# Kernel optimization log

Hardware: AMD Instinct MI355X
Metric: run time of the kernel (lower is better)

Reference implementation:

```python
import jax, jax.numpy as jnp
import numpy as np

MARKET_DIM, VELOCITY_DIM, AGENT_STATE_DIM = 20, 10, 10
RUNNER_DIM, POSITION_DIM, MAX_RUNNERS = 24, 8, 30
RUNNER_INPUT_DIM = RUNNER_DIM + POSITION_DIM            # 32
MARKET_TOTAL_DIM = MARKET_DIM + VELOCITY_DIM + AGENT_STATE_DIM  # 40
OBS_DIM = MARKET_DIM + VELOCITY_DIM + MAX_RUNNERS * RUNNER_DIM + AGENT_STATE_DIM + MAX_RUNNERS * POSITION_DIM  # 1000
TD_IDX = MARKET_DIM + (VELOCITY_DIM - 4)                # 26
B, T = 256, 64
MLP_H, LSTM_H = 128, 256
LSTM_IN = MLP_H + 2 * MLP_H                             # 384


def setup_inputs() -> dict:
    key = jax.random.key(0)
    ks = jax.random.split(key, 32)

    def w(k, o, i):
        return (jax.random.normal(k, (o, i), jnp.float32) / np.sqrt(i)).astype(jnp.float32)

    z = lambda n: jnp.zeros((n,), jnp.float32)
    return dict(
        obs=jax.random.normal(ks[0], (B, T, OBS_DIM), jnp.float32),
        # runner encoder: 32 -> 128 -> 128 -> 128
        re_w0=w(ks[1], MLP_H, RUNNER_INPUT_DIM), re_b0=z(MLP_H),
        re_w1=w(ks[2], MLP_H, MLP_H), re_b1=z(MLP_H),
        re_w2=w(ks[3], MLP_H, MLP_H), re_b2=z(MLP_H),
        # market encoder: 40 -> 128 -> 128 -> 128
        me_w0=w(ks[4], MLP_H, MARKET_TOTAL_DIM), me_b0=z(MLP_H),
        me_w1=w(ks[5], MLP_H, MLP_H), me_b1=z(MLP_H),
        me_w2=w(ks[6], MLP_H, MLP_H), me_b2=z(MLP_H),
        # TimeLSTM cell (single layer)
        W_ih=w(ks[7], 4 * LSTM_H, LSTM_IN), b_ih=z(4 * LSTM_H),
        W_hh=w(ks[8], 4 * LSTM_H, LSTM_H),
        W_dt=jnp.zeros((LSTM_H,), jnp.float32),
        # actor head: 384 -> 128 -> 2
        a_w0=w(ks[9], MLP_H, MLP_H + LSTM_H), a_b0=z(MLP_H),
        a_w1=w(ks[10], 2, MLP_H) * 0.01, a_b1=z(2),
        # critic head: 256 -> 128 -> 1
        c_w0=w(ks[11], MLP_H, LSTM_H), c_b0=z(MLP_H),
        c_w1=w(ks[12], 1, MLP_H), c_b1=z(1),
        log_std=jnp.zeros((MAX_RUNNERS * 2,), jnp.float32),
    )


def _mlp3(x, w0, b0, w1, b1, w2, b2):
    x = jax.nn.relu(x @ w0.T + b0)
    x = jax.nn.relu(x @ w1.T + b1)
    return x @ w2.T + b2


def _mlp2(x, w0, b0, w1, b1):
    return jax.nn.relu(x @ w0.T + b0) @ w1.T + b1


def reference(obs,
              re_w0, re_b0, re_w1, re_b1, re_w2, re_b2,
              me_w0, me_b0, me_w1, me_b1, me_w2, me_b2,
              W_ih, b_ih, W_hh, W_dt,
              a_w0, a_b0, a_w1, a_b1,
              c_w0, c_b0, c_w1, c_b1,
              log_std):
    b, t, _ = obs.shape
    of = obs.reshape(b * t, -1)
    market = of[:, :MARKET_DIM]
    vel = of[:, MARKET_DIM:MARKET_DIM + VELOCITY_DIM]
    rs = MARKET_DIM + VELOCITY_DIM
    re_ = rs + MAX_RUNNERS * RUNNER_DIM
    runners = of[:, rs:re_].reshape(b * t, MAX_RUNNERS, RUNNER_DIM)
    agent = of[:, re_:re_ + AGENT_STATE_DIM]
    ps = re_ + AGENT_STATE_DIM
    pos = of[:, ps:ps + MAX_RUNNERS * POSITION_DIM].reshape(b * t, MAX_RUNNERS, POSITION_DIM)

    market_feats = jnp.concatenate([market, vel, agent], axis=-1)        # (BT, 40)
    runner_feats = jnp.concatenate([runners, pos], axis=-1)              # (BT, R, 32)

    market_emb = _mlp3(market_feats, me_w0, me_b0, me_w1, me_b1, me_w2, me_b2)  # (BT, 128)
    runner_embs = _mlp3(runner_feats, re_w0, re_b0, re_w1, re_b1, re_w2, re_b2)  # (BT, R, 128)
    r_mean = runner_embs.mean(axis=1)
    r_max = runner_embs.max(axis=1)

    lstm_in = jnp.concatenate([market_emb, r_mean, r_max], axis=-1).reshape(b, t, LSTM_IN)
    dt = of[:, TD_IDX].reshape(b, t)

    h0 = jnp.zeros((b, LSTM_H), obs.dtype)
    c0 = jnp.zeros_like(h0)

    def step(hc, xs):
        h, c = hc
        x, d = xs                                           # (B, 384), (B,)
        gates = x @ W_ih.T + b_ih + h @ W_hh.T              # (B, 4H)
        i, f, g, o = jnp.split(gates, 4, axis=-1)
        f = f + W_dt * d[:, None]                           # time-modulated forget gate
        i, f, o = jax.nn.sigmoid(i), jax.nn.sigmoid(f), jax.nn.sigmoid(o)
        g = jnp.tanh(g)
        c_new = f * c + i * g
        h_new = o * jnp.tanh(c_new)
        return (h_new, c_new), None

    (h, c), _ = jax.lax.scan(step, (h0, c0), (lstm_in.transpose(1, 0, 2), dt.T))
    lstm_out = h  # layer_norm disabled -> identity

    runner_last = runner_embs.reshape(b, t, MAX_RUNNERS, MLP_H)[:, -1]   # (B, R, 128)
    actor_in = jnp.concatenate(
        [runner_last, jnp.broadcast_to(lstm_out[:, None, :], (b, MAX_RUNNERS, LSTM_H))], axis=-1)
    action_mean = _mlp2(actor_in, a_w0, a_b0, a_w1, a_b1).reshape(b, MAX_RUNNERS * 2)
    action_log_std = jnp.broadcast_to(log_std, action_mean.shape)
    value = _mlp2(lstm_out, c_w0, c_b0, c_w1, c_b1)                      # (B, 1)
    return action_mean, action_log_std, value, h, c
```

## Files before the change

kernel.cpp:

```cpp
#include <hip/hip_runtime.h>
#include <hip/hip_bf16.h>
#include <math.h>

#define Bn 256
#define Tn 64
#define OBSD 1000
#define NR 30
#define HD 128
#define LH 256
#define LIN 384
#define TDI 26

#define AM_OFF 0
#define ALS_OFF 15360
#define V_OFF 30720
#define H_OFF 30976
#define C_OFF 96512

typedef unsigned short u16;
typedef short bf16x8 __attribute__((ext_vector_type(8)));
typedef float f32x4 __attribute__((ext_vector_type(4)));

__device__ __forceinline__ float sigm(float x){ return 1.f/(1.f+__expf(-x)); }
__device__ __forceinline__ float tanhfast(float x){
    float ax = fabsf(x);
    float e = __expf(2.f*ax);
    float t = 1.f - 2.f/(e+1.f);
    return copysignf(t, x);
}

__device__ __forceinline__ u16 f2b(float f){
    union { __hip_bfloat16 h; u16 u; } cv;
    cv.h = __float2bfloat16(f);
    return cv.u;
}

__device__ __forceinline__ bf16x8 ld_b128_sys(const u16* p){
    bf16x8 r;
    asm volatile("global_load_dwordx4 %0, %1, off sc0 sc1"
                 : "=v"(r) : "v"(p) : "memory");
    return r;
}
__device__ __forceinline__ void st_b16_sys(u16* p, unsigned v){
    asm volatile("global_store_short %0, %1, off sc0 sc1"
                 :: "v"(p), "v"(v) : "memory");
}

#define MFMA(a,b,c) __builtin_amdgcn_mfma_f32_16x16x32_bf16(a,b,c,0,0,0)

__device__ __forceinline__ void pack_one(
    const float* __restrict__ src, u16* __restrict__ dst,
    int N, int K, int Kpad, int t)
{
    if (t >= N*Kpad) return;
    int j = t / Kpad, k = t - j*Kpad;
    float v = (k < K) ? src[j*K + k] : 0.f;
    int ntile = j>>4, jr = j&15, kc = k>>5, ko = k&31;
    int lane = ((ko>>3)<<4) | jr, elem = ko&7;
    int KC = Kpad>>5;
    dst[(size_t)(((ntile*KC + kc)*64) + lane)*8 + elem] = f2b(v);
}

__device__ __forceinline__ void pack_gi_one(
    const float* __restrict__ src, u16* __restrict__ dst, int K, int t)
{
    int KC = K >> 5;
    if (t >= 1024*K) return;
    int n = t / K, k = t - n*K;
    int nt = n>>4, jr = n&15;
    int jg = nt>>2, g = nt&3;
    float v = src[(size_t)(g*256 + jg*16 + jr)*K + k];
    int kc = k>>5, ko = k&31;
    int lane = ((ko>>3)<<4) | jr, e = ko&7;
    dst[(size_t)(((nt*KC + kc)*64) + lane)*8 + e] = f2b(v);
}

__global__ __launch_bounds__(256) void k_setup(
    const float* __restrict__ re_w0, u16* __restrict__ pw0,
    const float* __restrict__ re_w1, u16* __restrict__ pw1,
    const float* __restrict__ re_w2, u16* __restrict__ pw2,
    const float* __restrict__ me_w0, u16* __restrict__ pm0,
    const float* __restrict__ me_w1, u16* __restrict__ pm1,
    const float* __restrict__ me_w2, u16* __restrict__ pm2,
    const float* __restrict__ W_ih,  u16* __restrict__ pwih,
    const float* __restrict__ W_hh,  u16* __restrict__ pwhh,
    const float* __restrict__ obs,   float* __restrict__ dtv,
    unsigned int* __restrict__ flags)
{
    int blk = blockIdx.x, tid = threadIdx.x;
    if (blk < 16){            pack_one(re_w0, pw0, 128, 32, 32,  blk*256 + tid); }
    else if (blk < 80){       pack_one(re_w1, pw1, 128,128,128, (blk-16)*256 + tid); }
    else if (blk < 144){      pack_one(re_w2, pw2, 128,128,128, (blk-80)*256 + tid); }
    else if (blk < 176){      pack_one(me_w0, pm0, 128, 40, 64, (blk-144)*256 + tid); }
    else if (blk < 240){      pack_one(me_w1, pm1, 128,128,128, (blk-176)*256 + tid); }
    else if (blk < 304){      pack_one(me_w2, pm2, 128,128,128, (blk-240)*256 + tid); }
    else if (blk < 1840){     pack_gi_one(W_ih, pwih, 384, (blk-304)*256 + tid); }
    else if (blk < 2864){     pack_gi_one(W_hh, pwhh, 256, (blk-1840)*256 + tid); }
    else if (blk < 2928){
        int idx = (blk-2864)*256 + tid;
        int b = idx >> 6, t = idx & 63;
        dtv[t*256 + b] = obs[(size_t)idx*OBSD + TDI];
    } else {
        flags[(blk-2928)*256 + tid] = 0u;
    }
}

__global__ __launch_bounds__(256) void k_embed_market(
    const float* __restrict__ obs,
    const u16* __restrict__ pw0, const float* __restrict__ re_b0,
    const u16* __restrict__ pw1, const float* __restrict__ re_b1,
    const u16* __restrict__ pw2, const float* __restrict__ re_b2,
    const u16* __restrict__ pm0, const float* __restrict__ me_b0,
    const u16* __restrict__ pm1, const float* __restrict__ me_b1,
    const u16* __restrict__ pm2, const float* __restrict__ me_b2,
    u16* __restrict__ li_bf, float* __restrict__ runner_last)
{
    __shared__ __align__(16) u16 smem[19968];
    __shared__ float bsf[384];

    int blk = blockIdx.x, tid = threadIdx.x;
    int lane = tid & 63, wv = tid >> 6;
    int lr = lane & 15, lk = lane >> 4;
    f32x4 zero = {0.f,0.f,0.f,0.f};

    if (blk < 8192){
        u16* xr   = smem;
        u16* act1 = smem + 2560;
        u16* act2 = smem + 11264;
        float* bs0 = bsf, *bs1 = bsf+128, *bs2 = bsf+256;

        int bt0 = blk*2;

        for (int idx=tid; idx<2048; idx+=256){
            int r = idx>>5, k = idx&31;
            int sb = r>>5, rr = r&31;
            const float* row = obs + (size_t)(bt0+sb)*OBSD;
            float v = 0.f;
            if (rr < 30) v = (k<24) ? row[30 + rr*24 + k] : row[760 + rr*8 + (k-24)];
            xr[r*40 + k] = f2b(v);
        }
        if (tid < 128){ bs0[tid]=re_b0[tid]; bs1[tid]=re_b1[tid]; bs2[tid]=re_b2[tid]; }
        __syncthreads();

        f32x4 d[4][2];

        {
            bf16x8 a0[4];
            #pragma unroll
            for (int m=0;m<4;m++) a0[m] = *(const bf16x8*)(xr + (m*16+lr)*40 + lk*8);
            #pragma unroll
            for (int ns=0; ns<2; ns++){
                int n = 2*wv + ns;
                bf16x8 b = *(const bf16x8*)(pw0 + (size_t)(n*64 + lane)*8);
                #pragma unroll
                for (int m=0;m<4;m++) d[m][ns] = MFMA(a0[m], b, zero);
            }
        }
        #pragma unroll
        for (int m=0;m<4;m++)
            #pragma unroll
            for (int ns=0;ns<2;ns++){
                int col = (2*wv+ns)*16 + lr;
                float bias = bs0[col];
                #pragma unroll
                for (int r=0;r<4;r++)
                    act1[(m*16+lk*4+r)*136 + col] = f2b(fmaxf(d[m][ns][r] + bias, 0.f));
            }
        __syncthreads();

        #pragma unroll
        for (int m=0;m<4;m++)
            #pragma unroll
            for (int ns=0;ns<2;ns++) d[m][ns] = zero;
        #pragma unroll
        for (int kc=0; kc<4; kc++){
            bf16x8 am[4];
            #pragma unroll
            for (int m=0;m<4;m++) am[m] = *(const bf16x8*)(act1 + (m*16+lr)*136 + kc*32 + lk*8);
            #pragma unroll
            for (int ns=0; ns<2; ns++){
                int n = 2*wv + ns;
                bf16x8 b = *(const bf16x8*)(pw1 + (size_t)((n*4 + kc)*64 + lane)*8);
                #pragma unroll
                for (int m=0;m<4;m++) d[m][ns] = MFMA(am[m], b, d[m][ns]);
            }
        }
        #pragma unroll
        for (int m=0;m<4;m++)
            #pragma unroll
            for (int ns=0;ns<2;ns++){
                int col = (2*wv+ns)*16 + lr;
                float bias = bs1[col];
                #pragma unroll
                for (int r=0;r<4;r++)
                    act2[(m*16+lk*4+r)*136 + col] = f2b(fmaxf(d[m][ns][r] + bias, 0.f));
            }
        __syncthreads();

        #pragma unroll
        for (int m=0;m<4;m++)
            #pragma unroll
            for (int ns=0;ns<2;ns++) d[m][ns] = zero;
        #pragma unroll
        for (int kc=0; kc<4; kc++){
            bf16x8 am[4];
            #pragma unroll
            for (int m=0;m<4;m++) am[m] = *(const bf16x8*)(act2 + (m*16+lr)*136 + kc*32 + lk*8);
            #pragma unroll
            for (int ns=0; ns<2; ns++){
                int n = 2*wv + ns;
                bf16x8 b = *(const bf16x8*)(pw2 + (size_t)((n*4 + kc)*64 + lane)*8);
                #pragma unroll
                for (int m=0;m<4;m++) d[m][ns] = MFMA(am[m], b, d[m][ns]);
            }
        }

        u16* li0 = li_bf + (size_t)bt0*LIN;
        u16* li1 = li_bf + (size_t)(bt0+1)*LIN;
        bool last1 = (((bt0+1) & 63) == 63);
        int bb1 = (bt0+1) >> 6;

        #pragma unroll
        for (int ns=0; ns<2; ns++){
            int col = (2*wv+ns)*16 + lr;
            float bias = bs2[col];
            float vals[4][4];
            float s0=0.f, m0=-3.4e38f, s1=0.f, m1=-3.4e38f;
            #pragma unroll
            for (int m=0;m<4;m++)
                #pragma unroll
                for (int r=0;r<4;r++){
                    int rw = m*16 + lk*4 + r;
                    float v = d[m][ns][r] + bias;
                    vals[m][r] = v;
                    if (m < 2){
                        bool ok = rw < 30;
                        s0 += ok ? v : 0.f;
                        m0 = fmaxf(m0, ok ? v : -3.4e38f);
                    } else {
                        bool ok = (rw-32) < 30;
                        s1 += ok ? v : 0.f;
                        m1 = fmaxf(m1, ok ? v : -3.4e38f);
                    }
                }
            s0 += __shfl_xor(s0, 16); s0 += __shfl_xor(s0, 32);
            m0 = fmaxf(m0, __shfl_xor(m0, 16)); m0 = fmaxf(m0, __shfl_xor(m0, 32));
            s1 += __shfl_xor(s1, 16); s1 += __shfl_xor(s1, 32);
            m1 = fmaxf(m1, __shfl_xor(m1, 16)); m1 = fmaxf(m1, __shfl_xor(m1, 32));
            if (lk == 0){
                li0[128 + col] = f2b(s0 * (1.0f/30.0f));
                li0[256 + col] = f2b(m0);
            }
            if (lk == 1){
                li1[128 + col] = f2b(s1 * (1.0f/30.0f));
                li1[256 + col] = f2b(m1);
            }
            if (last1){
                #pragma unroll
                for (int m=2;m<4;m++)
                    #pragma unroll
                    for (int r=0;r<4;r++){
                        int rw = m*16 + lk*4 + r - 32;
                        if (rw < 30) runner_last[(size_t)bb1*3840 + rw*128 + col] = vals[m][r];
                    }
            }
        }
    } else {
        u16* xm  = smem;
        u16* ma1 = smem + 2304;
        u16* ma2 = smem + 6656;
        float* bs0 = bsf, *bs1 = bsf+128, *bs2 = bsf+256;

        int bt0 = (blk - 8192)*32;
        for (int idx=tid; idx<2048; idx+=256){
            int r = idx>>6, k = idx&63;
            const float* row = obs + (size_t)(bt0+r)*OBSD;
            float v = 0.f;
            if (k < 30) v = row[k];
            else if (k < 40) v = row[720 + k];
            xm[r*72 + k] = f2b(v);
        }
        if (tid < 128){ bs0[tid]=me_b0[tid]; bs1[tid]=me_b1[tid]; bs2[tid]=me_b2[tid]; }
        __syncthreads();

        f32x4 d[2][2];

        #pragma unroll
        for (int m=0;m<2;m++)
            #pragma unroll
            for (int ns=0;ns<2;ns++) d[m][ns] = zero;
        #pragma unroll
        for (int kc=0; kc<2; kc++){
            bf16x8 a0 = *(const bf16x8*)(xm + lr*72      + kc*32 + lk*8);
            bf16x8 a1 = *(const bf16x8*)(xm + (16+lr)*72 + kc*32 + lk*8);
            #pragma unroll
            for (int ns=0; ns<2; ns++){
                int n = 2*wv + ns;
                bf16x8 b = *(const bf16x8*)(pm0 + (size_t)((n*2 + kc)*64 + lane)*8);
                d[0][ns] = MFMA(a0, b, d[0][ns]);
                d[1][ns] = MFMA(a1, b, d[1][ns]);
            }
        }
        #pragma unroll
        for (int m=0;m<2;m++)
            #pragma unroll
            for (int ns=0;ns<2;ns++){
                int col = (2*wv+ns)*16 + lr;
                float bias = bs0[col];
                #pragma unroll
                for (int r=0;r<4;r++){
                    int rw = m*16 + lk*4 + r;
                    ma1[rw*136 + col] = f2b(fmaxf(d[m][ns][r] + bias, 0.f));
                }
            }
        __syncthreads();

        #pragma unroll
        for (int m=0;m<2;m++)
            #pragma unroll
            for (int ns=0;ns<2;ns++) d[m][ns] = zero;
        #pragma unroll
        for (int kc=0; kc<4; kc++){
            bf16x8 a0 = *(const bf16x8*)(ma1 + lr*136      + kc*32 + lk*8);
            bf16x8 a1 = *(const bf16x8*)(ma1 + (16+lr)*136 + kc*32 + lk*8);
            #pragma unroll
            for (int ns=0; ns<2; ns++){
                int n = 2*wv + ns;
                bf16x8 b = *(const bf16x8*)(pm1 + (size_t)((n*4 + kc)*64 + lane)*8);
                d[0][ns] = MFMA(a0, b, d[0][ns]);
                d[1][ns] = MFMA(a1, b, d[1][ns]);
            }
        }
        #pragma unroll
        for (int m=0;m<2;m++)
            #pragma unroll
            for (int ns=0;ns<2;ns++){
                int col = (2*wv+ns)*16 + lr;
                float bias = bs1[col];
                #pragma unroll
                for (int r=0;r<4;r++){
                    int rw = m*16 + lk*4 + r;
                    ma2[rw*136 + col] = f2b(fmaxf(d[m][ns][r] + bias, 0.f));
                }
            }
        __syncthreads();

        #pragma unroll
        for (int m=0;m<2;m++)
            #pragma unroll
            for (int ns=0;ns<2;ns++) d[m][ns] = zero;
        #pragma unroll
        for (int kc=0; kc<4; kc++){
            bf16x8 a0 = *(const bf16x8*)(ma2 + lr*136      + kc*32 + lk*8);
            bf16x8 a1 = *(const bf16x8*)(ma2 + (16+lr)*136 + kc*32 + lk*8);
            #pragma unroll
            for (int ns=0; ns<2; ns++){
                int n = 2*wv + ns;
                bf16x8 b = *(const bf16x8*)(pm2 + (size_t)((n*4 + kc)*64 + lane)*8);
                d[0][ns] = MFMA(a0, b, d[0][ns]);
                d[1][ns] = MFMA(a1, b, d[1][ns]);
            }
        }
        #pragma unroll
        for (int m=0;m<2;m++)
            #pragma unroll
            for (int ns=0;ns<2;ns++){
                int col = (2*wv+ns)*16 + lr;
                float bias = bs2[col];
                #pragma unroll
                for (int r=0;r<4;r++){
                    int rw = m*16 + lk*4 + r;
                    li_bf[(size_t)(bt0+rw)*LIN + col] = f2b(d[m][ns][r] + bias);
                }
            }
    }
}

__global__ __launch_bounds__(256) void k_xw(
    const u16* __restrict__ A, const u16* __restrict__ pwih,
    const float* __restrict__ b_ih, float* __restrict__ xw)
{
    __shared__ __align__(16) u16 bsh[48*512];

    int tid = threadIdx.x;
    int lane = tid & 63, wv = tid >> 6;
    int lr = lane & 15, lk = lane >> 4;
    int r0 = blockIdx.x*128 + wv*32;

    bf16x8 a[2][12];
    #pragma unroll
    for (int m=0;m<2;m++)
        #pragma unroll
        for (int kc=0;kc<12;kc++)
            a[m][kc] = *(const bf16x8*)(A + (size_t)(r0+m*16+lr)*384 + kc*32 + lk*8);

    for (int jg=0; jg<16; jg++){
        {
            const bf16x8* src = (const bf16x8*)(pwih + (size_t)jg*48*512);
            bf16x8* dst = (bf16x8*)bsh;
            #pragma unroll
            for (int i=0;i<12;i++)
                dst[tid + i*256] = src[tid + i*256];
        }
        __syncthreads();

        f32x4 acc[2][4];
        #pragma unroll
        for (int g=0; g<4; g++){
            float bias = b_ih[g*256 + jg*16 + lr];
            f32x4 v = {bias,bias,bias,bias};
            acc[0][g]=v; acc[1][g]=v;
        }
        #pragma unroll
        for (int kc=0; kc<12; kc++){
            bf16x8 b0 = *(const bf16x8*)(bsh + (size_t)((0*12+kc)*64+lane)*8);
            bf16x8 b1 = *(const bf16x8*)(bsh + (size_t)((1*12+kc)*64+lane)*8);
            bf16x8 b2 = *(const bf16x8*)(bsh + (size_t)((2*12+kc)*64+lane)*8);
            bf16x8 b3 = *(const bf16x8*)(bsh + (size_t)((3*12+kc)*64+lane)*8);
            #pragma unroll
            for (int m=0;m<2;m++){
                acc[m][0] = MFMA(a[m][kc], b0, acc[m][0]);
                acc[m][1] = MFMA(a[m][kc], b1, acc[m][1]);
                acc[m][2] = MFMA(a[m][kc], b2, acc[m][2]);
                acc[m][3] = MFMA(a[m][kc], b3, acc[m][3]);
            }
        }
        #pragma unroll
        for (int m=0;m<2;m++)
            #pragma unroll
            for (int r=0;r<4;r++){
                int row = r0 + m*16 + lk*4 + r;
                int trow = (row & 63)*256 + (row >> 6);
                float4 pk;
                pk.x = acc[m][0][r]; pk.y = acc[m][1][r];
                pk.z = acc[m][2][r]; pk.w = acc[m][3][r];
                *(float4*)(xw + ((size_t)trow*256 + jg*16 + lr)*4) = pk;
            }
        __syncthreads();
    }
}

__global__ __launch_bounds__(256,1) void k_lstm_pair(
    const float* __restrict__ xw, const u16* __restrict__ pwhh,
    const float* __restrict__ W_dt, const float* __restrict__ dtv,
    u16* __restrict__ hb0, u16* __restrict__ hb1,
    float* __restrict__ hout, float* __restrict__ cout,
    unsigned int* __restrict__ flags)
{
    int tid = threadIdx.x;
    int lane = tid & 63, wv = tid >> 6;
    int lr = lane & 15, lk = lane >> 4;
    int blk = blockIdx.x;
    int p = blk >> 1, hf = blk & 1;
    int bb0 = p*16;
    int jg0 = hf*8 + wv*2;

    bf16x8 bfr[2][4][8];
    #pragma unroll
    for (int jl=0;jl<2;jl++)
        #pragma unroll
        for (int g=0;g<4;g++)
            #pragma unroll
            for (int kc=0;kc<8;kc++)
                bfr[jl][g][kc] = *(const bf16x8*)(pwhh + (size_t)((((jg0+jl)*4+g)*8+kc)*64+lane)*8);

    float wdt0 = W_dt[jg0*16 + lr];
    float wdt1 = W_dt[(jg0+1)*16 + lr];

    float cst[2][4] = {{0.f,0.f,0.f,0.f},{0.f,0.f,0.f,0.f}};
    bf16x8 a[8];
    #pragma unroll
    for (int kc=0;kc<8;kc++) a[kc] = (bf16x8)(short)0;

    int bth = bb0 + lk*4;

    float4 xwn[2][4];
    #pragma unroll
    for (int jl=0;jl<2;jl++)
        #pragma unroll
        for (int r=0;r<4;r++)
            xwn[jl][r] = *(const float4*)(xw + ((size_t)(bth+r)*256 + (jg0+jl)*16 + lr)*4);
    float4 dtn = *(const float4*)(dtv + bth);

    f32x4 acc[2][4];
    #pragma unroll
    for (int jl=0;jl<2;jl++){
        f32x4 v0, v1, v2, v3;
        #pragma unroll
        for (int r=0;r<4;r++){
            v0[r] = xwn[jl][r].x; v1[r] = xwn[jl][r].y;
            v2[r] = xwn[jl][r].z; v3[r] = xwn[jl][r].w;
        }
        acc[jl][0] = v0; acc[jl][1] = v1; acc[jl][2] = v2; acc[jl][3] = v3;
    }

    unsigned int* myflag   = &flags[blk*64];
    unsigned int* partflag = &flags[(blk^1)*64];

    for (int t=0; t<64; t++){
        asm volatile("s_waitcnt vmcnt(0)" ::: "memory");
        __builtin_amdgcn_sched_barrier(0);

        #pragma unroll
        for (int kc=0; kc<8; kc++){
            #pragma unroll
            for (int jl=0;jl<2;jl++){
                acc[jl][0] = MFMA(a[kc], bfr[jl][0][kc], acc[jl][0]);
                acc[jl][1] = MFMA(a[kc], bfr[jl][1][kc], acc[jl][1]);
                acc[jl][2] = MFMA(a[kc], bfr[jl][2][kc], acc[jl][2]);
                acc[jl][3] = MFMA(a[kc], bfr[jl][3][kc], acc[jl][3]);
            }
        }

        u16* hw = (t&1) ? hb1 : hb0;
        #pragma unroll
        for (int jl=0;jl<2;jl++){
            float wdt = jl ? wdt1 : wdt0;
            int jcol = (jg0+jl)*16 + lr;
            #pragma unroll
            for (int r=0;r<4;r++){
                float dd = (r==0)?dtn.x:(r==1)?dtn.y:(r==2)?dtn.z:dtn.w;
                float gi = sigm(acc[jl][0][r]);
                float gf = sigm(acc[jl][1][r] + wdt*dd);
                float gg = tanhfast(acc[jl][2][r]);
                float go = sigm(acc[jl][3][r]);
                float cn = fmaf(gf, cst[jl][r], gi*gg);
                cst[jl][r] = cn;
                float hv = go * tanhfast(cn);
                if (t < 63){
                    st_b16_sys(hw + (size_t)(bth+r)*256 + jcol, (unsigned)f2b(hv));
                } else {
                    hout[(size_t)(bth+r)*256 + jcol] = hv;
                    cout[(size_t)(bth+r)*256 + jcol] = cn;
                }
            }
        }

        if (t < 63){
            asm volatile("s_waitcnt vmcnt(0)" ::: "memory");
            __syncthreads();
            if (tid == 0)
                __hip_atomic_store(myflag, (unsigned)(t+1),
                                   __ATOMIC_RELAXED, __HIP_MEMORY_SCOPE_SYSTEM);

            #pragma unroll
            for (int jl=0;jl<2;jl++)
                #pragma unroll
                for (int r=0;r<4;r++)
                    xwn[jl][r] = *(const float4*)(xw + ((size_t)((t+1)*256 + bth+r)*256 + (jg0+jl)*16 + lr)*4);
            dtn = *(const float4*)(dtv + (t+1)*256 + bth);

            if (lane == 0){
                while (__hip_atomic_load(partflag, __ATOMIC_RELAXED,
                                         __HIP_MEMORY_SCOPE_SYSTEM) < (unsigned)(t+1)) {}
            }
            __builtin_amdgcn_wave_barrier();

            const u16* hr = (t&1) ? hb1 : hb0;
            #pragma unroll
            for (int kc=0; kc<8; kc++)
                a[kc] = ld_b128_sys(hr + (size_t)(bb0+lr)*256 + kc*32 + lk*8);

            #pragma unroll
            for (int jl=0;jl<2;jl++){
                f32x4 v0, v1, v2, v3;
                #pragma unroll
                for (int r=0;r<4;r++){
                    v0[r] = xwn[jl][r].x; v1[r] = xwn[jl][r].y;
                    v2[r] = xwn[jl][r].z; v3[r] = xwn[jl][r].w;
                }
                acc[jl][0] = v0; acc[jl][1] = v1; acc[jl][2] = v2; acc[jl][3] = v3;
            }
        }
    }
}

__device__ __forceinline__ void dense30(
    const float* in, int istride,
    const float* __restrict__ W, int wstride, int K,
    const float* __restrict__ bias, const float* extra,
    float* outp, int ostride, bool relu, int j, int rh)
{
    float acc[15];
    #pragma unroll
    for (int i=0;i<15;i++) acc[i]=0.f;
    const float* w = W + j*wstride;
    for (int k=0;k<K;k+=4){
        float4 wv = *(const float4*)(w+k);
        #pragma unroll
        for (int i=0;i<15;i++){
            float4 xv = *(const float4*)(in + (rh+2*i)*istride + k);
            acc[i] = fmaf(wv.x,xv.x,acc[i]);
            acc[i] = fmaf(wv.y,xv.y,acc[i]);
            acc[i] = fmaf(wv.z,xv.z,acc[i]);
            acc[i] = fmaf(wv.w,xv.w,acc[i]);
        }
    }
    float bb = bias[j] + (extra ? extra[j] : 0.f);
    #pragma unroll
    for (int i=0;i<15;i++){
        float v = acc[i]+bb;
        outp[(rh+2*i)*ostride+j] = relu ? fmaxf(v,0.f) : v;
    }
}

__device__ __forceinline__ float dense1(
    const float* in, const float* __restrict__ W,
    const float* __restrict__ bias, int K, int j)
{
    const float* w = W + j*K;
    float s = 0.f;
    for (int k=0;k<K;k+=4){
        float4 wv = *(const float4*)(w+k);
        float4 xv = *(const float4*)(in+k);
        s = fmaf(wv.x,xv.x,s); s = fmaf(wv.y,xv.y,s);
        s = fmaf(wv.z,xv.z,s); s = fmaf(wv.w,xv.w,s);
    }
    return s + bias[j];
}

__global__ __launch_bounds__(256) void k_heads(
    const float* __restrict__ h, const float* __restrict__ cbuf,
    const float* __restrict__ rl,
    const float* __restrict__ a_w0, const float* __restrict__ a_b0,
    const float* __restrict__ a_w1, const float* __restrict__ a_b1,
    const float* __restrict__ c_w0, const float* __restrict__ c_b0,
    const float* __restrict__ c_w1, const float* __restrict__ c_b1,
    const float* __restrict__ log_std,
    float* __restrict__ out)
{
    __shared__ __align__(16) float hv[LH];
    __shared__ __align__(16) float rls[NR][HD];
    __shared__ __align__(16) float hid[NR][HD];
    __shared__ __align__(16) float dot2[HD];
    __shared__ __align__(16) float red[128];

    int b = blockIdx.x, tid = threadIdx.x;
    hv[tid] = h[b*LH + tid];
    for (int idx=tid; idx<NR*HD; idx+=256) rls[idx>>7][idx&127] = rl[(size_t)b*NR*HD + idx];
    __syncthreads();

    if (tid < 128){
        const float* w = a_w0 + tid*LIN + HD;
        float s = 0.f;
        for (int k=0;k<LH;k+=4){
            float4 wv = *(const float4*)(w+k);
            s = fmaf(wv.x,hv[k],s); s = fmaf(wv.y,hv[k+1],s);
            s = fmaf(wv.z,hv[k+2],s); s = fmaf(wv.w,hv[k+3],s);
        }
        dot2[tid] = s;
    }
    __syncthreads();

    int j = tid & 127, rh = tid >> 7;
    dense30(&rls[0][0], HD, a_w0, LIN, HD, a_b0, dot2, &hid[0][0], HD, true, j, rh);
    __syncthreads();

    if (tid < 60){
        int r = tid >> 1, o = tid & 1;
        const float* w = a_w1 + o*HD;
        float s = a_b1[o];
        for (int k=0;k<HD;k++) s = fmaf(hid[r][k], w[k], s);
        out[AM_OFF + b*60 + tid] = s;
        out[ALS_OFF + b*60 + tid] = log_std[tid];
    }

    float term = 0.f;
    if (tid < 128) term = fmaxf(dense1(hv, c_w0, c_b0, LH, tid), 0.f) * c_w1[tid];
    if (tid < 128) red[tid] = term;
    __syncthreads();
    for (int s2=64; s2>0; s2>>=1){
        if (tid < s2) red[tid] += red[tid+s2];
        __syncthreads();
    }
    if (tid == 0) out[V_OFF + b] = red[0] + c_b1[0];

    out[H_OFF + b*LH + tid] = hv[tid];
    out[C_OFF + b*LH + tid] = cbuf[b*LH + tid];
}

extern "C" void kernel_launch(void* const* d_in, const int* in_sizes, int n_in,
                              void* d_out, int out_size, void* d_ws, size_t ws_size,
                              hipStream_t stream)
{
    const float* obs   = (const float*)d_in[0];
    const float* re_w0 = (const float*)d_in[1];
    const float* re_b0 = (const float*)d_in[2];
    const float* re_w1 = (const float*)d_in[3];
    const float* re_b1 = (const float*)d_in[4];
    const float* re_w2 = (const float*)d_in[5];
    const float* re_b2 = (const float*)d_in[6];
    const float* me_w0 = (const float*)d_in[7];
    const float* me_b0 = (const float*)d_in[8];
    const float* me_w1 = (const float*)d_in[9];
    const float* me_b1 = (const float*)d_in[10];
    const float* me_w2 = (const float*)d_in[11];
    const float* me_b2 = (const float*)d_in[12];
    const float* W_ih  = (const float*)d_in[13];
    const float* b_ih  = (const float*)d_in[14];
    const float* W_hh  = (const float*)d_in[15];
    const float* W_dt  = (const float*)d_in[16];
    const float* a_w0  = (const float*)d_in[17];
    const float* a_b0  = (const float*)d_in[18];
    const float* a_w1  = (const float*)d_in[19];
    const float* a_b1  = (const float*)d_in[20];
    const float* c_w0  = (const float*)d_in[21];
    const float* c_b0  = (const float*)d_in[22];
    const float* c_w1  = (const float*)d_in[23];
    const float* c_b1  = (const float*)d_in[24];
    const float* lstd  = (const float*)d_in[25];
    float* out = (float*)d_out;

    float* ws = (float*)d_ws;
    size_t off = 0;
    float* xw4  = ws + off; off += (size_t)16384*1024;
    float* hout = ws + off; off += (size_t)Bn*LH;
    float* cb   = ws + off; off += (size_t)Bn*LH;
    float* rl   = ws + off; off += (size_t)Bn*NR*HD;
    float* dtv  = ws + off; off += (size_t)16384;
    unsigned int* flags = (unsigned int*)(ws + off); off += 2048;

    u16* us = (u16*)(ws + off);
    size_t uo = 0;
    u16* li_bf = us + uo; uo += (size_t)16384*LIN;
    u16* pw0   = us + uo; uo += 128*32;
    u16* pw1   = us + uo; uo += 128*128;
    u16* pw2   = us + uo; uo += 128*128;
    u16* pm0   = us + uo; uo += 128*64;
    u16* pm1   = us + uo; uo += 128*128;
    u16* pm2   = us + uo; uo += 128*128;
    u16* pwih  = us + uo; uo += (size_t)1024*384;
    u16* pwhh  = us + uo; uo += (size_t)1024*256;
    u16* hb0   = us + uo; uo += (size_t)Bn*LH;
    u16* hb1   = us + uo; uo += (size_t)Bn*LH;

    k_setup<<<2936, 256, 0, stream>>>(re_w0, pw0, re_w1, pw1, re_w2, pw2,
                                      me_w0, pm0, me_w1, pm1, me_w2, pm2,
                                      W_ih, pwih, W_hh, pwhh, obs, dtv, flags);

    k_embed_market<<<8704, 256, 0, stream>>>(obs,
                                      pw0, re_b0, pw1, re_b1, pw2, re_b2,
                                      pm0, me_b0, pm1, me_b1, pm2, me_b2,
                                      li_bf, rl);

    k_xw<<<128, 256, 0, stream>>>(li_bf, pwih, b_ih, xw4);

    k_lstm_pair<<<32, 256, 0, stream>>>(xw4, pwhh, W_dt, dtv, hb0, hb1,
                                        hout, cb, flags);

    k_heads<<<256, 256, 0, stream>>>(hout, cb, rl,
        a_w0, a_b0, a_w1, a_b1, c_w0, c_b0, c_w1, c_b1, lstd, out);
}
```

Before: 448.5 us.

## Fuse input projection into LSTM kernel with per-timestep producer/consumer flags

Merges the x·W_ih projection kernel and the recurrent LSTM kernel into one launch. The first 32 blocks run the recurrence, and the remaining 128 blocks compute the projection one timestep (and batch half) at a time, publishing progress through ordered counters. The recurrence blocks spin on those counters before loading each step's projection. This lets the serial recurrence start while later timesteps are still being projected, removing a kernel boundary. The cost is system-scope loads and stores and spin-waits, and it depends on all 160 blocks being co-resident.

```diff
diff --git a/kernel.cpp b/kernel.cpp
--- a/kernel.cpp
+++ b/kernel.cpp
@@ -43,6 +43,16 @@
 }
 __device__ __forceinline__ void st_b16_sys(u16* p, unsigned v){
     asm volatile("global_store_short %0, %1, off sc0 sc1"
+                 :: "v"(p), "v"(v) : "memory");
+}
+__device__ __forceinline__ f32x4 ld_f32x4_sys(const float* p){
+    f32x4 r;
+    asm volatile("global_load_dwordx4 %0, %1, off sc0 sc1"
+                 : "=v"(r) : "v"(p) : "memory");
+    return r;
+}
+__device__ __forceinline__ void st_f32x4_sys(float* p, f32x4 v){
+    asm volatile("global_store_dwordx4 %0, %1, off sc0 sc1"
                  :: "v"(p), "v"(v) : "memory");
 }
 
@@ -376,81 +386,91 @@
     }
 }
 
-__global__ __launch_bounds__(256) void k_xw(
+__global__ __launch_bounds__(256,1) void k_xwlstm(
     const u16* __restrict__ A, const u16* __restrict__ pwih,
-    const float* __restrict__ b_ih, float* __restrict__ xw)
+    const float* __restrict__ b_ih, float* __restrict__ xw,
+    const u16* __restrict__ pwhh, const float* __restrict__ W_dt,
+    const float* __restrict__ dtv,
+    u16* __restrict__ hb0, u16* __restrict__ hb1,
+    float* __restrict__ hout, float* __restrict__ cout,
+    unsigned int* __restrict__ flags)
 {
     __shared__ __align__(16) u16 bsh[48*512];
 
+    int blk = blockIdx.x;
     int tid = threadIdx.x;
     int lane = tid & 63, wv = tid >> 6;
     int lr = lane & 15, lk = lane >> 4;
-    int r0 = blockIdx.x*128 + wv*32;
-
-    bf16x8 a[2][12];
-    #pragma unroll
-    for (int m=0;m<2;m++)
-        #pragma unroll
-        for (int kc=0;kc<12;kc++)
-            a[m][kc] = *(const bf16x8*)(A + (size_t)(r0+m*16+lr)*384 + kc*32 + lk*8);
-
-    for (int jg=0; jg<16; jg++){
-        {
-            const bf16x8* src = (const bf16x8*)(pwih + (size_t)jg*48*512);
-            bf16x8* dst = (bf16x8*)bsh;
-            #pragma unroll
-            for (int i=0;i<12;i++)
-                dst[tid + i*256] = src[tid + i*256];
-        }
+
+    if (blk >= 32){
+        int tb = blk - 32;
+        int t = tb >> 1, half = tb & 1;
+        int b0 = half*128 + wv*32;
+
+        bf16x8 a[2][12];
+        #pragma unroll
+        for (int m=0;m<2;m++)
+            #pragma unroll
+            for (int kc=0;kc<12;kc++)
+                a[m][kc] = *(const bf16x8*)(A + ((size_t)(b0+m*16+lr)*64 + t)*384 + kc*32 + lk*8);
+
+        for (int jg=0; jg<16; jg++){
+            {
+                const bf16x8* src = (const bf16x8*)(pwih + (size_t)jg*48*512);
+                bf16x8* dst = (bf16x8*)bsh;
+                #pragma unroll
+                for (int i=0;i<12;i++)
+                    dst[tid + i*256] = src[tid + i*256];
+            }
+            __syncthreads();
+
+            f32x4 acc[2][4];
+            #pragma unroll
+            for (int g=0; g<4; g++){
+                float bias = b_ih[g*256 + jg*16 + lr];
+                f32x4 v = {bias,bias,bias,bias};
+                acc[0][g]=v; acc[1][g]=v;
+            }
+            #pragma unroll
+            for (int kc=0; kc<12; kc++){
+                bf16x8 b0v = *(const bf16x8*)(bsh + (size_t)((0*12+kc)*64+lane)*8);
+                bf16x8 b1v = *(const bf16x8*)(bsh + (size_t)((1*12+kc)*64+lane)*8);
+                bf16x8 b2v = *(const bf16x8*)(bsh + (size_t)((2*12+kc)*64+lane)*8);
+                bf16x8 b3v = *(const bf16x8*)(bsh + (size_t)((3*12+kc)*64+lane)*8);
+                #pragma unroll
+                for (int m=0;m<2;m++){
+                    acc[m][0] = MFMA(a[m][kc], b0v, acc[m][0]);
+                    acc[m][1] = MFMA(a[m][kc], b1v, acc[m][1]);
+                    acc[m][2] = MFMA(a[m][kc], b2v, acc[m][2]);
+                    acc[m][3] = MFMA(a[m][kc], b3v, acc[m][3]);
+                }
+            }
+            #pragma unroll
+            for (int m=0;m<2;m++)
+                #pragma unroll
+                for (int r=0;r<4;r++){
+                    int b = b0 + m*16 + lk*4 + r;
+                    int trow = t*256 + b;
+                    f32x4 pk;
+                    pk[0] = acc[m][0][r]; pk[1] = acc[m][1][r];
+                    pk[2] = acc[m][2][r]; pk[3] = acc[m][3][r];
+                    st_f32x4_sys(xw + ((size_t)trow*256 + jg*16 + lr)*4, pk);
+                }
+            __syncthreads();
+        }
+
+        asm volatile("s_waitcnt vmcnt(0)" ::: "memory");
         __syncthreads();
-
-        f32x4 acc[2][4];
-        #pragma unroll
-        for (int g=0; g<4; g++){
-            float bias = b_ih[g*256 + jg*16 + lr];
-            f32x4 v = {bias,bias,bias,bias};
-            acc[0][g]=v; acc[1][g]=v;
-        }
-        #pragma unroll
-        for (int kc=0; kc<12; kc++){
-            bf16x8 b0 = *(const bf16x8*)(bsh + (size_t)((0*12+kc)*64+lane)*8);
-            bf16x8 b1 = *(const bf16x8*)(bsh + (size_t)((1*12+kc)*64+lane)*8);
-            bf16x8 b2 = *(const bf16x8*)(bsh + (size_t)((2*12+kc)*64+lane)*8);
-            bf16x8 b3 = *(const bf16x8*)(bsh + (size_t)((3*12+kc)*64+lane)*8);
-            #pragma unroll
-            for (int m=0;m<2;m++){
-                acc[m][0] = MFMA(a[m][kc], b0, acc[m][0]);
-                acc[m][1] = MFMA(a[m][kc], b1, acc[m][1]);
-                acc[m][2] = MFMA(a[m][kc], b2, acc[m][2]);
-                acc[m][3] = MFMA(a[m][kc], b3, acc[m][3]);
-            }
-        }
-        #pragma unroll
-        for (int m=0;m<2;m++)
-            #pragma unroll
-            for (int r=0;r<4;r++){
-                int row = r0 + m*16 + lk*4 + r;
-                int trow = (row & 63)*256 + (row >> 6);
-                float4 pk;
-                pk.x = acc[m][0][r]; pk.y = acc[m][1][r];
-                pk.z = acc[m][2][r]; pk.w = acc[m][3][r];
-                *(float4*)(xw + ((size_t)trow*256 + jg*16 + lr)*4) = pk;
-            }
-        __syncthreads();
-    }
-}
-
-__global__ __launch_bounds__(256,1) void k_lstm_pair(
-    const float* __restrict__ xw, const u16* __restrict__ pwhh,
-    const float* __restrict__ W_dt, const float* __restrict__ dtv,
-    u16* __restrict__ hb0, u16* __restrict__ hb1,
-    float* __restrict__ hout, float* __restrict__ cout,
-    unsigned int* __restrict__ flags)
-{
-    int tid = threadIdx.x;
-    int lane = tid & 63, wv = tid >> 6;
-    int lr = lane & 15, lk = lane >> 4;
-    int blk = blockIdx.x;
+        if (tid == 0){
+            unsigned* cnt = &flags[2048 + half*128];
+            while (__hip_atomic_load(cnt, __ATOMIC_RELAXED, __HIP_MEMORY_SCOPE_SYSTEM)
+                   != (unsigned)t) {}
+            __hip_atomic_store(cnt, (unsigned)(t+1),
+                               __ATOMIC_RELAXED, __HIP_MEMORY_SCOPE_SYSTEM);
+        }
+        return;
+    }
+
     int p = blk >> 1, hf = blk & 1;
     int bb0 = p*16;
     int jg0 = hf*8 + wv*2;
@@ -474,13 +494,25 @@
 
     int bth = bb0 + lk*4;
 
-    float4 xwn[2][4];
+    const unsigned* xcnt = &flags[2048 + ((p >= 8) ? 128 : 0)];
+    unsigned seen = 0;
+
+    while (seen < 1u){
+        unsigned v = 0;
+        if (lane == 0)
+            v = __hip_atomic_load(xcnt, __ATOMIC_RELAXED, __HIP_MEMORY_SCOPE_SYSTEM);
+        v = __shfl(v, 0);
+        seen = v;
+    }
+
+    f32x4 xwn[2][4];
     #pragma unroll
     for (int jl=0;jl<2;jl++)
         #pragma unroll
         for (int r=0;r<4;r++)
-            xwn[jl][r] = *(const float4*)(xw + ((size_t)(bth+r)*256 + (jg0+jl)*16 + lr)*4);
+            xwn[jl][r] = ld_f32x4_sys(xw + ((size_t)(bth+r)*256 + (jg0+jl)*16 + lr)*4);
     float4 dtn = *(const float4*)(dtv + bth);
+    asm volatile("s_waitcnt vmcnt(0)" ::: "memory");
 
     f32x4 acc[2][4];
     #pragma unroll
@@ -488,8 +520,8 @@
         f32x4 v0, v1, v2, v3;
         #pragma unroll
         for (int r=0;r<4;r++){
-            v0[r] = xwn[jl][r].x; v1[r] = xwn[jl][r].y;
-            v2[r] = xwn[jl][r].z; v3[r] = xwn[jl][r].w;
+            v0[r] = xwn[jl][r][0]; v1[r] = xwn[jl][r][1];
+            v2[r] = xwn[jl][r][2]; v3[r] = xwn[jl][r][3];
         }
         acc[jl][0] = v0; acc[jl][1] = v1; acc[jl][2] = v2; acc[jl][3] = v3;
     }
@@ -543,11 +575,19 @@
                 __hip_atomic_store(myflag, (unsigned)(t+1),
                                    __ATOMIC_RELAXED, __HIP_MEMORY_SCOPE_SYSTEM);
 
+            while (seen < (unsigned)(t+2)){
+                unsigned v = 0;
+                if (lane == 0)
+                    v = __hip_atomic_load(xcnt, __ATOMIC_RELAXED, __HIP_MEMORY_SCOPE_SYSTEM);
+                v = __shfl(v, 0);
+                seen = v;
+            }
+
             #pragma unroll
             for (int jl=0;jl<2;jl++)
                 #pragma unroll
                 for (int r=0;r<4;r++)
-                    xwn[jl][r] = *(const float4*)(xw + ((size_t)((t+1)*256 + bth+r)*256 + (jg0+jl)*16 + lr)*4);
+                    xwn[jl][r] = ld_f32x4_sys(xw + ((size_t)((t+1)*256 + bth+r)*256 + (jg0+jl)*16 + lr)*4);
             dtn = *(const float4*)(dtv + (t+1)*256 + bth);
 
             if (lane == 0){
@@ -561,13 +601,14 @@
             for (int kc=0; kc<8; kc++)
                 a[kc] = ld_b128_sys(hr + (size_t)(bb0+lr)*256 + kc*32 + lk*8);
 
+            asm volatile("s_waitcnt vmcnt(8)" ::: "memory");
             #pragma unroll
             for (int jl=0;jl<2;jl++){
                 f32x4 v0, v1, v2, v3;
                 #pragma unroll
                 for (int r=0;r<4;r++){
-                    v0[r] = xwn[jl][r].x; v1[r] = xwn[jl][r].y;
-                    v2[r] = xwn[jl][r].z; v3[r] = xwn[jl][r].w;
+                    v0[r] = xwn[jl][r][0]; v1[r] = xwn[jl][r][1];
+                    v2[r] = xwn[jl][r][2]; v3[r] = xwn[jl][r][3];
                 }
                 acc[jl][0] = v0; acc[jl][1] = v1; acc[jl][2] = v2; acc[jl][3] = v3;
             }
@@ -718,7 +759,7 @@
     float* cb   = ws + off; off += (size_t)Bn*LH;
     float* rl   = ws + off; off += (size_t)Bn*NR*HD;
     float* dtv  = ws + off; off += (size_t)16384;
-    unsigned int* flags = (unsigned int*)(ws + off); off += 2048;
+    unsigned int* flags = (unsigned int*)(ws + off); off += 2304;
 
     u16* us = (u16*)(ws + off);
     size_t uo = 0;
@@ -734,7 +775,7 @@
     u16* hb0   = us + uo; uo += (size_t)Bn*LH;
     u16* hb1   = us + uo; uo += (size_t)Bn*LH;
 
-    k_setup<<<2936, 256, 0, stream>>>(re_w0, pw0, re_w1, pw1, re_w2, pw2,
+    k_setup<<<2937, 256, 0, stream>>>(re_w0, pw0, re_w1, pw1, re_w2, pw2,
                                       me_w0, pm0, me_w1, pm1, me_w2, pm2,
                                       W_ih, pwih, W_hh, pwhh, obs, dtv, flags);
 
@@ -743,10 +784,9 @@
                                       pm0, me_b0, pm1, me_b1, pm2, me_b2,
                                       li_bf, rl);
 
-    k_xw<<<128, 256, 0, stream>>>(li_bf, pwih, b_ih, xw4);
-
-    k_lstm_pair<<<32, 256, 0, stream>>>(xw4, pwhh, W_dt, dtv, hb0, hb1,
-                                        hout, cb, flags);
+    k_xwlstm<<<160, 256, 0, stream>>>(li_bf, pwih, b_ih, xw4,
+                                      pwhh, W_dt, dtv, hb0, hb1,
+                                      hout, cb, flags);
 
     k_heads<<<256, 256, 0, stream>>>(hout, cb, rl,
         a_w0, a_b0, a_w1, a_b1, c_w0, c_b0, c_w1, c_b1, lstd, out);
```

After: 440.6 us. Within noise of the previous version (-1.8%).
